# Performance work log

Hardware: AMD Instinct MI355X
Metric: run time of the kernel (lower is better)

Reference implementation:

```python
import jax, jax.numpy as jnp
import numpy as np

B, NPG, DEG = 256, 256, 8        # graphs, nodes/graph, avg degree
IN_C, HID, OUT_C = 64, 64, 64
N = B * NPG                      # 65536 nodes
E = N * DEG                      # 524288 edges
K = NPG // 2                     # ASAP ratio=0.5 -> 128 kept nodes per graph


def setup_inputs() -> dict:
    key = jax.random.key(0)
    ks = jax.random.split(key, 12)
    x = jax.random.normal(ks[0], (N, IN_C), jnp.float32)
    # within-graph random edges, no self loops (ASAP adds remaining self loops itself)
    g = jnp.arange(E) // (NPG * DEG)
    src_l = jax.random.randint(ks[1], (E,), 0, NPG)
    off = jax.random.randint(ks[2], (E,), 1, NPG)
    dst_l = (src_l + off) % NPG
    edge_index = jnp.stack([src_l + g * NPG, dst_l + g * NPG]).astype(jnp.int32)
    batch = (jnp.arange(N) // NPG).astype(jnp.int32)
    def lin(k, fi, fo):
        return jax.random.normal(k, (fi, fo), jnp.float32) / np.sqrt(fi)
    return {
        "x": x, "edge_index": edge_index, "batch": batch,
        "W1": lin(ks[3], IN_C, HID), "b1": jnp.zeros((HID,), jnp.float32),
        "lin_W": lin(ks[4], HID, HID), "lin_b": jnp.zeros((HID,), jnp.float32),
        "att_W": lin(ks[5], 2 * HID, 1), "att_b": jnp.zeros((1,), jnp.float32),
        "le1_W": lin(ks[6], HID, 1), "le1_b": jnp.zeros((1,), jnp.float32),
        "le2_W": lin(ks[7], HID, 1),
        "le3_W": lin(ks[8], HID, 1), "le3_b": jnp.zeros((1,), jnp.float32),
        "W2": lin(ks[9], HID, OUT_C), "b2": jnp.zeros((OUT_C,), jnp.float32),
    }


def reference(x, edge_index, batch, W1, b1, lin_W, lin_b, att_W, att_b,
              le1_W, le1_b, le2_W, le3_W, le3_b, W2, b2):
    src, dst = edge_index[0], edge_index[1]
    dt = x.dtype

    # ---- conv1: GCNConv(in, hid) with self loops + symmetric norm ----
    h = x @ W1
    deg = jnp.zeros((N,), dt).at[dst].add(1.0) + 1.0  # +1 self loop
    dinv = jax.lax.rsqrt(deg)
    coef = dinv[src] * dinv[dst]
    h1 = jax.ops.segment_sum(h[src] * coef[:, None], dst, N) \
         + h * (dinv * dinv)[:, None] + b1
    h1 = jax.nn.relu(h1)  # dropout is identity at inference

    # ---- ASAPooling(hid, ratio=0.5): add remaining self loops ----
    sl = jnp.arange(N)
    srcF = jnp.concatenate([src, sl])
    dstF = jnp.concatenate([dst, sl])

    x_pool_j = h1[srcF]                                   # [Ef, HID]
    x_q = jax.ops.segment_max(x_pool_j, dstF, N)          # master-node max
    x_q = (x_q @ lin_W + lin_b)[dstF]
    s = (jnp.concatenate([x_q, x_pool_j], axis=-1) @ att_W + att_b)[:, 0]
    s = jax.nn.leaky_relu(s, 0.2)
    # segment softmax over edges grouped by target
    smax = jax.ops.segment_max(s, dstF, N)
    e = jnp.exp(s - smax[dstF])
    score = e / (jax.ops.segment_sum(e, dstF, N) + 1e-16)[dstF]
    xnew = jax.ops.segment_sum(h1[srcF] * score[:, None], dstF, N)

    # fitness = sigmoid(LEConv(xnew, edges_with_self_loops))
    # LEConv: out_i = sum_{j->i}(lin1(x_j) - lin2(x_i)) + lin3(x_i)
    a = xnew @ le1_W + le1_b
    b2_ = xnew @ le2_W
    degF = jnp.zeros((N,), dt).at[dstF].add(1.0)
    fit = jax.ops.segment_sum(a[srcF], dstF, N)[:, 0] - degF * b2_[:, 0] \
          + (xnew @ le3_W + le3_b)[:, 0]
    fitness = jax.nn.sigmoid(fit)

    # top-k (ratio=0.5) per graph; equal contiguous graphs -> static shapes
    _, topi = jax.lax.top_k(fitness.reshape(B, NPG), K)   # [B, K]
    perm = (topi + jnp.arange(B)[:, None] * NPG).reshape(-1)
    x_sel = xnew[perm] * fitness[perm][:, None]           # [B*K, HID]

    # graph coarsening: A' = S^T A S (dense per graph), diag removed
    g_e = dstF // NPG
    sL = srcF - g_e * NPG
    dL = dstF - g_e * NPG
    A = jnp.zeros((B, NPG, NPG), dt).at[g_e, sL, dL].add(1.0)
    S = jnp.zeros((B, NPG, NPG), dt).at[g_e, sL, dL].add(score)
    Ssel = jnp.take_along_axis(S, topi[:, None, :], axis=2)   # [B, NPG, K]
    AS = jnp.einsum('bij,bjk->bik', A, Ssel)                  # A @ S
    A2 = jnp.einsum('bji,bjk->bik', Ssel, AS)                 # S^T (A S) -> [B,K,K]
    A2 = A2 * (1.0 - jnp.eye(K, dtype=dt))                    # remove_diag

    # ---- conv2: GCNConv(hid, out); returned edge_weight is discarded in
    # the original forward, so edges are binary (nnz of A') + self loops ----
    M = (A2 > 0).astype(dt) + jnp.eye(K, dtype=dt)            # [B, src, dst]
    h2 = (x_sel @ W2).reshape(B, K, OUT_C)
    deg2 = M.sum(axis=1)                                      # in-degree per target
    d2 = jax.lax.rsqrt(deg2)
    Mn = M * d2[:, :, None] * d2[:, None, :]
    out2 = jnp.einsum('bsd,bsf->bdf', Mn, h2) + b2            # [B, K, OUT_C]

    # ---- global_mean_pool over each graph's K kept nodes ----
    return out2.mean(axis=1)                                  # [B, OUT_C]
```

## Files before the change

kernel.cpp:

```cpp
#include <hip/hip_runtime.h>

#define NPGL 256
#define EPGL 2048
#define HIDD 64
#define KKEEP 128
#define NTH 1024

__device__ __forceinline__ int swz(int n, int c) {
  return (n << 6) + ((((c ^ n) ^ (n >> 4)) & 15) << 2);
}

__global__ void __launch_bounds__(NTH)
asap_fused(const float* __restrict__ x, const int* __restrict__ ei,
           const float* __restrict__ W1, const float* __restrict__ b1,
           const float* __restrict__ linW, const float* __restrict__ linb,
           const float* __restrict__ attW, const float* __restrict__ attb,
           const float* __restrict__ le1W, const float* __restrict__ le1b,
           const float* __restrict__ le2W,
           const float* __restrict__ le3W, const float* __restrict__ le3b,
           const float* __restrict__ W2, const float* __restrict__ b2,
           float* __restrict__ out, int Etot)
{
  const int g = blockIdx.x;
  const int tid = threadIdx.x;

  __shared__ __align__(16) float buf[NPGL * HIDD];
  __shared__ __align__(16) float mskf[4096];
  __shared__ unsigned short csrc[EPGL];
  __shared__ int rowst[NPGL + 1];
  __shared__ int cnt[NPGL];
  __shared__ float dinv_[NPGL];
  __shared__ float sA[NPGL], sB[NPGL];
  __shared__ float eself[NPGL];
  __shared__ float rsf[NPGL];
  __shared__ __align__(16) float esc[EPGL];
  __shared__ float u_[HIDD];
  __shared__ float wsum[HIDD];
  __shared__ int scanw[4];
  __shared__ float c0s;

  unsigned long long* Imask = (unsigned long long*)mskf;
  unsigned long long* Rmask = ((unsigned long long*)mskf) + 1024;
  unsigned long long* conn  = ((unsigned long long*)mskf) + 1536;
  int*   kept = (int*)(mskf + 3584);
  float* d2A  = mskf + 3712;
  float* cA   = mskf + 3840;

  const int ebase = g * EPGL;
  const int nbase = g * NPGL;

  if (tid < NPGL) cnt[tid] = 0;
  __syncthreads();

  int es[2], ed[2];
#pragma unroll
  for (int i = 0; i < 2; ++i) {
    const int e = tid + i * NTH;
    es[i] = ei[ebase + e] - nbase;
    ed[i] = ei[Etot + ebase + e] - nbase;
    atomicAdd(&cnt[ed[i]], 1);
  }

  __syncthreads();

  int vscan = 0;
  if (tid < NPGL) {
    vscan = cnt[tid];
#pragma unroll
    for (int off = 1; off < 64; off <<= 1) {
      const int up = __shfl_up(vscan, off, 64);
      if ((tid & 63) >= off) vscan += up;
    }
    if ((tid & 63) == 63) scanw[tid >> 6] = vscan;
  }
  __syncthreads();
  if (tid < NPGL) {
    int add = 0;
    const int w = tid >> 6;
    for (int ww = 0; ww < w; ++ww) add += scanw[ww];
    const int incl = vscan + add;
    rowst[tid + 1] = incl;
    cnt[tid] = incl - cnt[tid];
    if (tid == 0) rowst[0] = 0;
  }
  __syncthreads();

#pragma unroll
  for (int i = 0; i < 2; ++i) {
    const int p = atomicAdd(&cnt[ed[i]], 1);
    csrc[p] = (unsigned short)es[i];
  }
  if (tid < NPGL) {
    const int len = rowst[tid + 1] - rowst[tid];
    dinv_[tid] = rsqrtf((float)len + 1.0f);
  }
  if (tid < HIDD) {
    float a = 0.f;
    for (int f = 0; f < HIDD; ++f) a += linW[tid * HIDD + f] * attW[f];
    u_[tid] = a;
  }
  if (tid == 0) {
    float a = 0.f;
    for (int f = 0; f < HIDD; ++f) a += linb[f] * attW[f];
    c0s = a + attb[0];
  }
  {
    const float4* xg = (const float4*)(x + (size_t)nbase * HIDD);
#pragma unroll
    for (int ii = 0; ii < 4; ++ii) {
      const int i = tid + ii * NTH;
      const int r = i >> 4, c = i & 15;
      *(float4*)&buf[swz(r, c)] = xg[i];
    }
  }
  __syncthreads();

  {
    const int wv = tid >> 6;
    const int r  = ((wv & 3) << 6) + (tid & 63);
    const int fc = __builtin_amdgcn_readfirstlane(wv >> 2);
    const float* __restrict__ Wg = W1 + fc * 16;
    float4 acc[4];
#pragma unroll
    for (int c = 0; c < 4; ++c) acc[c] = make_float4(0.f, 0.f, 0.f, 0.f);
#pragma unroll
    for (int p = 0; p < 4; ++p) {
      float4 xa[4];
#pragma unroll
      for (int c = 0; c < 4; ++c) xa[c] = *(const float4*)&buf[swz(r, p * 4 + c)];
#pragma unroll
      for (int kk = 0; kk < 16; ++kk) {
        const int k = p * 16 + kk;
        const float xv = ((const float*)xa)[kk];
        const float* __restrict__ Wk = Wg + k * HIDD;
#pragma unroll
        for (int c = 0; c < 4; ++c) {
          const float4 w = *(const float4*)(Wk + c * 4);
          acc[c].x += xv * w.x; acc[c].y += xv * w.y;
          acc[c].z += xv * w.z; acc[c].w += xv * w.w;
        }
      }
    }
    __syncthreads();
#pragma unroll
    for (int c = 0; c < 4; ++c) *(float4*)&buf[swz(r, fc * 4 + c)] = acc[c];
  }
  __syncthreads();

  {
    const int d = tid >> 2, hh = tid & 3;
    const float dd = dinv_[d];
    const float sc_ = dd * dd;
    float4 acc[4];
#pragma unroll
    for (int j = 0; j < 4; ++j) {
      const int c = hh + 4 * j;
      const float4 hv = *(const float4*)&buf[swz(d, c)];
      const float4 bv = *(const float4*)&b1[4 * c];
      acc[j].x = hv.x * sc_ + bv.x; acc[j].y = hv.y * sc_ + bv.y;
      acc[j].z = hv.z * sc_ + bv.z; acc[j].w = hv.w * sc_ + bv.w;
    }
    const int s0 = rowst[d], s1 = rowst[d + 1];
    int it = s0;
    for (; it + 2 <= s1; it += 2) {
      const int sa_ = csrc[it], sb_ = csrc[it + 1];
      const float ca_ = dinv_[sa_] * dd, cb_ = dinv_[sb_] * dd;
#pragma unroll
      for (int j = 0; j < 4; ++j) {
        const float4 ha = *(const float4*)&buf[swz(sa_, hh + 4 * j)];
        const float4 hb = *(const float4*)&buf[swz(sb_, hh + 4 * j)];
        acc[j].x += ca_ * ha.x + cb_ * hb.x;
        acc[j].y += ca_ * ha.y + cb_ * hb.y;
        acc[j].z += ca_ * ha.z + cb_ * hb.z;
        acc[j].w += ca_ * ha.w + cb_ * hb.w;
      }
    }
    if (it < s1) {
      const int s = csrc[it];
      const float cf = dinv_[s] * dd;
#pragma unroll
      for (int j = 0; j < 4; ++j) {
        const float4 hv = *(const float4*)&buf[swz(s, hh + 4 * j)];
        acc[j].x += cf * hv.x; acc[j].y += cf * hv.y;
        acc[j].z += cf * hv.z; acc[j].w += cf * hv.w;
      }
    }
#pragma unroll
    for (int j = 0; j < 4; ++j) {
      acc[j].x = fmaxf(acc[j].x, 0.f); acc[j].y = fmaxf(acc[j].y, 0.f);
      acc[j].z = fmaxf(acc[j].z, 0.f); acc[j].w = fmaxf(acc[j].w, 0.f);
    }
    __syncthreads();
#pragma unroll
    for (int j = 0; j < 4; ++j) *(float4*)&buf[swz(d, hh + 4 * j)] = acc[j];
  }
  __syncthreads();

  {
    const int d = tid >> 2, hh = tid & 3;
    float4 mx[4];
    float sBp = 0.f;
#pragma unroll
    for (int j = 0; j < 4; ++j) {
      const int c = hh + 4 * j;
      const float4 hv = *(const float4*)&buf[swz(d, c)];
      mx[j] = hv;
      const float4 aw = *(const float4*)&attW[HIDD + 4 * c];
      sBp += hv.x * aw.x + hv.y * aw.y + hv.z * aw.z + hv.w * aw.w;
    }
    const int s0 = rowst[d], s1 = rowst[d + 1];
    int it = s0;
    for (; it + 2 <= s1; it += 2) {
      const int sa_ = csrc[it], sb_ = csrc[it + 1];
#pragma unroll
      for (int j = 0; j < 4; ++j) {
        const float4 ha = *(const float4*)&buf[swz(sa_, hh + 4 * j)];
        const float4 hb = *(const float4*)&buf[swz(sb_, hh + 4 * j)];
        mx[j].x = fmaxf(mx[j].x, fmaxf(ha.x, hb.x));
        mx[j].y = fmaxf(mx[j].y, fmaxf(ha.y, hb.y));
        mx[j].z = fmaxf(mx[j].z, fmaxf(ha.z, hb.z));
        mx[j].w = fmaxf(mx[j].w, fmaxf(ha.w, hb.w));
      }
    }
    if (it < s1) {
      const int s = csrc[it];
#pragma unroll
      for (int j = 0; j < 4; ++j) {
        const float4 hv = *(const float4*)&buf[swz(s, hh + 4 * j)];
        mx[j].x = fmaxf(mx[j].x, hv.x); mx[j].y = fmaxf(mx[j].y, hv.y);
        mx[j].z = fmaxf(mx[j].z, hv.z); mx[j].w = fmaxf(mx[j].w, hv.w);
      }
    }
    float sAp = 0.f;
#pragma unroll
    for (int j = 0; j < 4; ++j) {
      const float* uu = &u_[4 * (hh + 4 * j)];
      sAp += mx[j].x * uu[0] + mx[j].y * uu[1] + mx[j].z * uu[2] + mx[j].w * uu[3];
    }
    sAp += __shfl_xor(sAp, 1); sAp += __shfl_xor(sAp, 2);
    sBp += __shfl_xor(sBp, 1); sBp += __shfl_xor(sBp, 2);
    if (hh == 0) { sA[d] = c0s + sAp; sB[d] = sBp; }
  }
  __syncthreads();

  {
    const int d = tid >> 2, q = tid & 3;
    const float sa = sA[d];
    const int s0 = rowst[d], s1 = rowst[d + 1];
    float scS = sa + sB[d];
    scS = scS >= 0.f ? scS : 0.2f * scS;
    float mxv = scS;
    for (int it = s0 + q; it < s1; it += 4) {
      float sc = sa + sB[csrc[it]];
      sc = sc >= 0.f ? sc : 0.2f * sc;
      mxv = fmaxf(mxv, sc);
    }
    mxv = fmaxf(mxv, __shfl_xor(mxv, 1));
    mxv = fmaxf(mxv, __shfl_xor(mxv, 2));
    float sum = 0.f;
    for (int it = s0 + q; it < s1; it += 4) {
      float sc = sa + sB[csrc[it]];
      sc = sc >= 0.f ? sc : 0.2f * sc;
      const float e = __expf(sc - mxv);
      esc[it] = e;
      sum += e;
    }
    sum += __shfl_xor(sum, 1); sum += __shfl_xor(sum, 2);
    const float esf = __expf(scS - mxv);
    if (q == 0) {
      eself[d] = esf;
      rsf[d] = 1.0f / (esf + sum + 1e-16f);
    }
  }
  __syncthreads();

  {
    const int d = tid >> 2, hh = tid & 3;
    const float esf = eself[d];
    float4 acc[4];
#pragma unroll
    for (int j = 0; j < 4; ++j) {
      const float4 hv = *(const float4*)&buf[swz(d, hh + 4 * j)];
      acc[j].x = esf * hv.x; acc[j].y = esf * hv.y;
      acc[j].z = esf * hv.z; acc[j].w = esf * hv.w;
    }
    const int s0 = rowst[d], s1 = rowst[d + 1];
    int it = s0;
    for (; it + 2 <= s1; it += 2) {
      const int sa_ = csrc[it], sb_ = csrc[it + 1];
      const float ea = esc[it], eb = esc[it + 1];
#pragma unroll
      for (int j = 0; j < 4; ++j) {
        const float4 ha = *(const float4*)&buf[swz(sa_, hh + 4 * j)];
        const float4 hb = *(const float4*)&buf[swz(sb_, hh + 4 * j)];
        acc[j].x += ea * ha.x + eb * hb.x;
        acc[j].y += ea * ha.y + eb * hb.y;
        acc[j].z += ea * ha.z + eb * hb.z;
        acc[j].w += ea * ha.w + eb * hb.w;
      }
    }
    if (it < s1) {
      const int s = csrc[it];
      const float e = esc[it];
#pragma unroll
      for (int j = 0; j < 4; ++j) {
        const float4 hv = *(const float4*)&buf[swz(s, hh + 4 * j)];
        acc[j].x += e * hv.x; acc[j].y += e * hv.y;
        acc[j].z += e * hv.z; acc[j].w += e * hv.w;
      }
    }
    const float r = rsf[d];
#pragma unroll
    for (int j = 0; j < 4; ++j) {
      acc[j].x *= r; acc[j].y *= r; acc[j].z *= r; acc[j].w *= r;
    }
    __syncthreads();
#pragma unroll
    for (int j = 0; j < 4; ++j) *(float4*)&buf[swz(d, hh + 4 * j)] = acc[j];
  }
  __syncthreads();

  {
    const int n = tid >> 2, q = tid & 3;
    float av = 0.f, bv = 0.f, cv = 0.f;
#pragma unroll
    for (int j = 0; j < 4; ++j) {
      const int c = q + 4 * j;
      const float4 v = *(const float4*)&buf[swz(n, c)];
      const int k = c * 4;
      av += v.x * le1W[k] + v.y * le1W[k + 1] + v.z * le1W[k + 2] + v.w * le1W[k + 3];
      bv += v.x * le2W[k] + v.y * le2W[k + 1] + v.z * le2W[k + 2] + v.w * le2W[k + 3];
      cv += v.x * le3W[k] + v.y * le3W[k + 1] + v.z * le3W[k + 2] + v.w * le3W[k + 3];
    }
    av += __shfl_xor(av, 1); av += __shfl_xor(av, 2);
    bv += __shfl_xor(bv, 1); bv += __shfl_xor(bv, 2);
    cv += __shfl_xor(cv, 1); cv += __shfl_xor(cv, 2);
    if (q == 0) {
      sA[n] = av + le1b[0];
      sB[n] = bv;
      dinv_[n] = cv + le3b[0];
    }
  }
  __syncthreads();
  {
    const int d = tid >> 2, q = tid & 3;
    const int s0 = rowst[d], s1 = rowst[d + 1];
    float fp = 0.f;
    for (int it = s0 + q; it < s1; it += 4) fp += sA[csrc[it]];
    fp += __shfl_xor(fp, 1); fp += __shfl_xor(fp, 2);
    if (q == 0) {
      float f = sA[d] + fp;
      f -= (float)(s1 - s0 + 1) * sB[d];
      f += dinv_[d];
      float sg;
      if (f >= 0.f) sg = 1.f / (1.f + expf(-f));
      else { const float t = expf(f); sg = t / (1.f + t); }
      rsf[d] = sg;
    }
  }
  __syncthreads();

  {
    const int n = tid >> 2, q = tid & 3;
    const float fn = rsf[n];
    int r = 0;
    for (int m = q * 64; m < q * 64 + 64; ++m) {
      const float fm = rsf[m];
      r += ((fm > fn) || (fm == fn && m < n)) ? 1 : 0;
    }
    r += __shfl_xor(r, 1); r += __shfl_xor(r, 2);
    if (q == 0 && r < KKEEP) kept[r] = n;
  }
  __syncthreads();

  Imask[tid] = 0ull;
  __syncthreads();
  if (tid < NPGL) atomicOr(&Imask[tid * 4 + (tid >> 6)], 1ull << (tid & 63));
#pragma unroll
  for (int i = 0; i < 2; ++i)
    atomicOr(&Imask[ed[i] * 4 + (es[i] >> 6)], 1ull << (es[i] & 63));
  __syncthreads();

  if (tid < KKEEP * 4) {
    const int q = tid >> 2, w = tid & 3;
    const int kq = kept[q];
    unsigned long long acc = 0ull;
#pragma unroll
    for (int ww = 0; ww < 4; ++ww) {
      unsigned long long bits = Imask[kq * 4 + ww];
      while (bits) {
        const int m = (ww << 6) + __builtin_ctzll(bits);
        bits &= bits - 1;
        acc |= Imask[m * 4 + w];
      }
    }
    Rmask[q * 4 + w] = acc;
  }
  __syncthreads();
  if (tid < KKEEP * 2) conn[tid] = 0ull;
  __syncthreads();
  if (tid < KKEEP * 4) {
    const int p = tid >> 2, wb = tid & 3;
    const int kp = kept[p];
    const unsigned long long I0 = Imask[kp * 4 + 0], I1 = Imask[kp * 4 + 1],
                             I2 = Imask[kp * 4 + 2], I3 = Imask[kp * 4 + 3];
    unsigned long long bits = 0ull;
    for (int j = 0; j < 32; ++j) {
      const int q = wb * 32 + j;
      if (q == p) continue;
      const unsigned long long* R = &Rmask[q * 4];
      if ((I0 & R[0]) | (I1 & R[1]) | (I2 & R[2]) | (I3 & R[3]))
        bits |= 1ull << (q & 63);
    }
    atomicOr(&conn[p * 2 + (wb >> 1)], bits);
  }
  __syncthreads();

  if (tid < KKEEP) {
    const int q = tid;
    const int w = q >> 6;
    const unsigned long long bq = 1ull << (q & 63);
    int deg = 1;
    for (int p = 0; p < KKEEP; ++p) deg += (conn[p * 2 + w] & bq) ? 1 : 0;
    d2A[q] = rsqrtf((float)deg);
  }
  __syncthreads();
  if (tid < KKEEP) {
    const int s = tid;
    float acc = d2A[s];
#pragma unroll
    for (int w = 0; w < 2; ++w) {
      unsigned long long bits = conn[s * 2 + w];
      while (bits) {
        const int d = (w << 6) + __builtin_ctzll(bits);
        bits &= bits - 1;
        acc += d2A[d];
      }
    }
    cA[s] = d2A[s] * acc * rsf[kept[s]] * (1.0f / (float)KKEEP);
  }
  __syncthreads();

  {
    const int f = tid & 63, blk = tid >> 6;
    float p = 0.f;
    for (int j = 0; j < 8; ++j) {
      const int s = blk * 8 + j;
      const int ks = kept[s];
      const int off = (ks << 6) + (((((f >> 2) ^ ks) ^ (ks >> 4)) & 15) << 2) + (f & 3);
      p += cA[s] * buf[off];
    }
    esc[blk * 64 + f] = p;
  }
  __syncthreads();
  if (tid < HIDD) {
    float s = 0.f;
#pragma unroll
    for (int b = 0; b < 16; ++b) s += esc[b * 64 + tid];
    wsum[tid] = s;
  }
  __syncthreads();
  if (tid < HIDD) {
    float o = b2[tid];
    for (int k = 0; k < HIDD; ++k) o += wsum[k] * W2[k * HIDD + tid];
    out[(size_t)g * HIDD + tid] = o;
  }
}

extern "C" void kernel_launch(void* const* d_in, const int* in_sizes, int n_in,
                              void* d_out, int out_size, void* d_ws, size_t ws_size,
                              hipStream_t stream) {
  (void)n_in; (void)out_size; (void)d_ws; (void)ws_size;
  const float* x    = (const float*)d_in[0];
  const int*   ei   = (const int*)d_in[1];
  const float* W1   = (const float*)d_in[3];
  const float* b1   = (const float*)d_in[4];
  const float* linW = (const float*)d_in[5];
  const float* linb = (const float*)d_in[6];
  const float* attW = (const float*)d_in[7];
  const float* attb = (const float*)d_in[8];
  const float* le1W = (const float*)d_in[9];
  const float* le1b = (const float*)d_in[10];
  const float* le2W = (const float*)d_in[11];
  const float* le3W = (const float*)d_in[12];
  const float* le3b = (const float*)d_in[13];
  const float* W2   = (const float*)d_in[14];
  const float* b2   = (const float*)d_in[15];
  const int Etot = in_sizes[1] / 2;
  const int nGraphs = 256;

  asap_fused<<<dim3(nGraphs), dim3(NTH), 0, stream>>>(
      x, ei, W1, b1, linW, linb, attW, attb, le1W, le1b, le2W, le3W, le3b,
      W2, b2, (float*)d_out, Etot);
}
```

Baseline: 58.20 us.

## Sort nodes by in-degree for wavefront load balance and fuse softmax with aggregation

Builds a per-graph permutation of nodes ordered by in-degree through a shared-memory histogram and prefix scan. The edge-iterating phases use it so each 64-lane wavefront handles nodes with similar degrees, which cuts divergence in the per-node edge loops. It also merges the attention softmax stage with the weighted aggregation stage, dropping the eself/rsf shared round-trip and one block barrier. The cost is an extra counting-sort pass with atomics and barriers, plus an indirect perm lookup in every phase.

```diff
diff --git a/kernel.cpp b/kernel.cpp
--- a/kernel.cpp
+++ b/kernel.cpp
@@ -31,13 +31,15 @@
   __shared__ int cnt[NPGL];
   __shared__ float dinv_[NPGL];
   __shared__ float sA[NPGL], sB[NPGL];
-  __shared__ float eself[NPGL];
   __shared__ float rsf[NPGL];
   __shared__ __align__(16) float esc[EPGL];
   __shared__ float u_[HIDD];
   __shared__ float wsum[HIDD];
   __shared__ int scanw[4];
   __shared__ float c0s;
+  __shared__ int perm[NPGL];
+  __shared__ int dhist[64];
+  __shared__ int dcur[64];
 
   unsigned long long* Imask = (unsigned long long*)mskf;
   unsigned long long* Rmask = ((unsigned long long*)mskf) + 1024;
@@ -50,6 +52,7 @@
   const int nbase = g * NPGL;
 
   if (tid < NPGL) cnt[tid] = 0;
+  if (tid >= NTH - 64) dhist[tid - (NTH - 64)] = 0;
   __syncthreads();
 
   int es[2], ed[2];
@@ -60,7 +63,6 @@
     ed[i] = ei[Etot + ebase + e] - nbase;
     atomicAdd(&cnt[ed[i]], 1);
   }
-
   __syncthreads();
 
   int vscan = 0;
@@ -93,6 +95,7 @@
   if (tid < NPGL) {
     const int len = rowst[tid + 1] - rowst[tid];
     dinv_[tid] = rsqrtf((float)len + 1.0f);
+    atomicAdd(&dhist[len < 63 ? len : 63], 1);
   }
   if (tid < HIDD) {
     float a = 0.f;
@@ -147,8 +150,26 @@
   }
   __syncthreads();
 
-  {
-    const int d = tid >> 2, hh = tid & 3;
+  if (tid < 64) {
+    const int v = dhist[tid];
+    int s = v;
+#pragma unroll
+    for (int off = 1; off < 64; off <<= 1) {
+      const int up = __shfl_up(s, off, 64);
+      if (tid >= off) s += up;
+    }
+    dcur[tid] = s - v;
+  }
+  __syncthreads();
+  if (tid < NPGL) {
+    const int len = rowst[tid + 1] - rowst[tid];
+    const int b = len < 63 ? len : 63;
+    perm[atomicAdd(&dcur[b], 1)] = tid;
+  }
+  __syncthreads();
+
+  {
+    const int d = perm[tid >> 2], hh = tid & 3;
     const float dd = dinv_[d];
     const float sc_ = dd * dd;
     float4 acc[4];
@@ -197,7 +218,7 @@
   __syncthreads();
 
   {
-    const int d = tid >> 2, hh = tid & 3;
+    const int d = perm[tid >> 2], hh = tid & 3;
     float4 mx[4];
     float sBp = 0.f;
 #pragma unroll
@@ -244,13 +265,13 @@
   __syncthreads();
 
   {
-    const int d = tid >> 2, q = tid & 3;
+    const int d = perm[tid >> 2], hh = tid & 3;
     const float sa = sA[d];
     const int s0 = rowst[d], s1 = rowst[d + 1];
     float scS = sa + sB[d];
     scS = scS >= 0.f ? scS : 0.2f * scS;
     float mxv = scS;
-    for (int it = s0 + q; it < s1; it += 4) {
+    for (int it = s0 + hh; it < s1; it += 4) {
       float sc = sa + sB[csrc[it]];
       sc = sc >= 0.f ? sc : 0.2f * sc;
       mxv = fmaxf(mxv, sc);
@@ -258,7 +279,7 @@
     mxv = fmaxf(mxv, __shfl_xor(mxv, 1));
     mxv = fmaxf(mxv, __shfl_xor(mxv, 2));
     float sum = 0.f;
-    for (int it = s0 + q; it < s1; it += 4) {
+    for (int it = s0 + hh; it < s1; it += 4) {
       float sc = sa + sB[csrc[it]];
       sc = sc >= 0.f ? sc : 0.2f * sc;
       const float e = __expf(sc - mxv);
@@ -267,16 +288,8 @@
     }
     sum += __shfl_xor(sum, 1); sum += __shfl_xor(sum, 2);
     const float esf = __expf(scS - mxv);
-    if (q == 0) {
-      eself[d] = esf;
-      rsf[d] = 1.0f / (esf + sum + 1e-16f);
-    }
-  }
-  __syncthreads();
-
-  {
-    const int d = tid >> 2, hh = tid & 3;
-    const float esf = eself[d];
+    const float rs = 1.0f / (esf + sum + 1e-16f);
+
     float4 acc[4];
 #pragma unroll
     for (int j = 0; j < 4; ++j) {
@@ -284,7 +297,6 @@
       acc[j].x = esf * hv.x; acc[j].y = esf * hv.y;
       acc[j].z = esf * hv.z; acc[j].w = esf * hv.w;
     }
-    const int s0 = rowst[d], s1 = rowst[d + 1];
     int it = s0;
     for (; it + 2 <= s1; it += 2) {
       const int sa_ = csrc[it], sb_ = csrc[it + 1];
@@ -309,10 +321,9 @@
         acc[j].z += e * hv.z; acc[j].w += e * hv.w;
       }
     }
-    const float r = rsf[d];
-#pragma unroll
-    for (int j = 0; j < 4; ++j) {
-      acc[j].x *= r; acc[j].y *= r; acc[j].z *= r; acc[j].w *= r;
+#pragma unroll
+    for (int j = 0; j < 4; ++j) {
+      acc[j].x *= rs; acc[j].y *= rs; acc[j].z *= rs; acc[j].w *= rs;
     }
     __syncthreads();
 #pragma unroll
@@ -343,7 +354,7 @@
   }
   __syncthreads();
   {
-    const int d = tid >> 2, q = tid & 3;
+    const int d = perm[tid >> 2], q = tid & 3;
     const int s0 = rowst[d], s1 = rowst[d + 1];
     float fp = 0.f;
     for (int it = s0 + q; it < s1; it += 4) fp += sA[csrc[it]];
```

Result: no change. 59.34 us (+1.9%).

## Fuse ASAP attention phases and remap to 16 lanes per node

Applied to the files above, without the earlier changes.

Each node is now handled by 16 lanes with one float4 per lane instead of 4 lanes with four float4s, so neighbour-row gathers read whole contiguous 256-byte rows from LDS. The attention score, softmax and weighted aggregation are merged into one phase, with the first eight neighbour rows cached in registers and reused. Per-edge GCN coefficients are computed once during CSR construction, and the adjacency bitmask build and the x load are moved earlier to overlap with other setup. The change also simplifies the LDS swizzle, stores source indices as bytes, and drops several barriers; in exchange it uses more registers and places a barrier inside a branch on the thread index.

```diff
diff --git a/kernel.cpp b/kernel.cpp
--- a/kernel.cpp
+++ b/kernel.cpp
@@ -1,4 +1,6 @@
 #include <hip/hip_runtime.h>
+
+typedef float f4 __attribute__((ext_vector_type(4)));
 
 #define NPGL 256
 #define EPGL 2048
@@ -7,7 +9,7 @@
 #define NTH 1024
 
 __device__ __forceinline__ int swz(int n, int c) {
-  return (n << 6) + ((((c ^ n) ^ (n >> 4)) & 15) << 2);
+  return (n << 6) + (((c ^ n) & 15) << 2);
 }
 
 __global__ void __launch_bounds__(NTH)
@@ -23,17 +25,18 @@
 {
   const int g = blockIdx.x;
   const int tid = threadIdx.x;
+  const int ln = tid & 15;
+  const int grp = tid >> 4;
 
   __shared__ __align__(16) float buf[NPGL * HIDD];
   __shared__ __align__(16) float mskf[4096];
-  __shared__ unsigned short csrc[EPGL];
+  __shared__ __align__(16) float esc[EPGL];
+  __shared__ unsigned char csrc[EPGL];
   __shared__ int rowst[NPGL + 1];
   __shared__ int cnt[NPGL];
   __shared__ float dinv_[NPGL];
   __shared__ float sA[NPGL], sB[NPGL];
-  __shared__ float eself[NPGL];
   __shared__ float rsf[NPGL];
-  __shared__ __align__(16) float esc[EPGL];
   __shared__ float u_[HIDD];
   __shared__ float wsum[HIDD];
   __shared__ int scanw[4];
@@ -49,6 +52,7 @@
   const int ebase = g * EPGL;
   const int nbase = g * NPGL;
 
+  ((unsigned long long*)mskf)[tid] = 0ull;
   if (tid < NPGL) cnt[tid] = 0;
   __syncthreads();
 
@@ -60,39 +64,36 @@
     ed[i] = ei[Etot + ebase + e] - nbase;
     atomicAdd(&cnt[ed[i]], 1);
   }
-
-  __syncthreads();
-
-  int vscan = 0;
+  {
+    const f4* xg = (const f4*)(x + (size_t)nbase * HIDD);
+#pragma unroll
+    for (int ii = 0; ii < 4; ++ii) {
+      const int i = tid + ii * NTH;
+      *(f4*)&buf[swz(i >> 4, i & 15)] = xg[i];
+    }
+  }
+  __syncthreads();
+
   if (tid < NPGL) {
-    vscan = cnt[tid];
+    const int myc = cnt[tid];
+    int vscan = myc;
 #pragma unroll
     for (int off = 1; off < 64; off <<= 1) {
       const int up = __shfl_up(vscan, off, 64);
       if ((tid & 63) >= off) vscan += up;
     }
     if ((tid & 63) == 63) scanw[tid >> 6] = vscan;
-  }
-  __syncthreads();
-  if (tid < NPGL) {
+    dinv_[tid] = rsqrtf((float)myc + 1.0f);
+    __syncthreads();
     int add = 0;
     const int w = tid >> 6;
     for (int ww = 0; ww < w; ++ww) add += scanw[ww];
     const int incl = vscan + add;
     rowst[tid + 1] = incl;
-    cnt[tid] = incl - cnt[tid];
+    cnt[tid] = incl - myc;
     if (tid == 0) rowst[0] = 0;
-  }
-  __syncthreads();
-
-#pragma unroll
-  for (int i = 0; i < 2; ++i) {
-    const int p = atomicAdd(&cnt[ed[i]], 1);
-    csrc[p] = (unsigned short)es[i];
-  }
-  if (tid < NPGL) {
-    const int len = rowst[tid + 1] - rowst[tid];
-    dinv_[tid] = rsqrtf((float)len + 1.0f);
+  } else {
+    __syncthreads();
   }
   if (tid < HIDD) {
     float a = 0.f;
@@ -104,15 +105,18 @@
     for (int f = 0; f < HIDD; ++f) a += linb[f] * attW[f];
     c0s = a + attb[0];
   }
-  {
-    const float4* xg = (const float4*)(x + (size_t)nbase * HIDD);
-#pragma unroll
-    for (int ii = 0; ii < 4; ++ii) {
-      const int i = tid + ii * NTH;
-      const int r = i >> 4, c = i & 15;
-      *(float4*)&buf[swz(r, c)] = xg[i];
-    }
-  }
+  __syncthreads();
+
+#pragma unroll
+  for (int i = 0; i < 2; ++i) {
+    const int p = atomicAdd(&cnt[ed[i]], 1);
+    csrc[p] = (unsigned char)es[i];
+    esc[p] = dinv_[es[i]] * dinv_[ed[i]];
+  }
+  if (tid < NPGL) atomicOr(&Imask[tid * 4 + (tid >> 6)], 1ull << (tid & 63));
+#pragma unroll
+  for (int i = 0; i < 2; ++i)
+    atomicOr(&Imask[ed[i] * 4 + (es[i] >> 6)], 1ull << (es[i] & 63));
   __syncthreads();
 
   {
@@ -120,222 +124,155 @@
     const int r  = ((wv & 3) << 6) + (tid & 63);
     const int fc = __builtin_amdgcn_readfirstlane(wv >> 2);
     const float* __restrict__ Wg = W1 + fc * 16;
-    float4 acc[4];
-#pragma unroll
-    for (int c = 0; c < 4; ++c) acc[c] = make_float4(0.f, 0.f, 0.f, 0.f);
+    f4 acc[4];
+#pragma unroll
+    for (int c = 0; c < 4; ++c) acc[c] = f4{0.f, 0.f, 0.f, 0.f};
 #pragma unroll
     for (int p = 0; p < 4; ++p) {
-      float4 xa[4];
-#pragma unroll
-      for (int c = 0; c < 4; ++c) xa[c] = *(const float4*)&buf[swz(r, p * 4 + c)];
+      f4 xa[4];
+#pragma unroll
+      for (int c = 0; c < 4; ++c) xa[c] = *(const f4*)&buf[swz(r, p * 4 + c)];
 #pragma unroll
       for (int kk = 0; kk < 16; ++kk) {
         const int k = p * 16 + kk;
         const float xv = ((const float*)xa)[kk];
         const float* __restrict__ Wk = Wg + k * HIDD;
 #pragma unroll
-        for (int c = 0; c < 4; ++c) {
-          const float4 w = *(const float4*)(Wk + c * 4);
-          acc[c].x += xv * w.x; acc[c].y += xv * w.y;
-          acc[c].z += xv * w.z; acc[c].w += xv * w.w;
+        for (int c = 0; c < 4; ++c)
+          acc[c] += xv * *(const f4*)(Wk + c * 4);
+      }
+    }
+    __syncthreads();
+#pragma unroll
+    for (int c = 0; c < 4; ++c) *(f4*)&buf[swz(r, fc * 4 + c)] = acc[c];
+  }
+  __syncthreads();
+
+  {
+    f4 hacc[4];
+#pragma unroll
+    for (int p = 0; p < 4; ++p) {
+      const int d = (p << 6) + grp;
+      const float dd = dinv_[d];
+      const f4 own = *(const f4*)&buf[swz(d, ln)];
+      const f4 bv = *(const f4*)&b1[ln * 4];
+      f4 a = own * (dd * dd) + bv;
+      const int s0 = rowst[d], s1 = rowst[d + 1];
+      int it = s0;
+      for (; it + 2 <= s1; it += 2) {
+        const int sa_ = csrc[it], sb_ = csrc[it + 1];
+        const float ca_ = esc[it], cb_ = esc[it + 1];
+        const f4 va = *(const f4*)&buf[swz(sa_, ln)];
+        const f4 vb = *(const f4*)&buf[swz(sb_, ln)];
+        a += ca_ * va + cb_ * vb;
+      }
+      if (it < s1) {
+        const int s = csrc[it];
+        a += esc[it] * *(const f4*)&buf[swz(s, ln)];
+      }
+      a = __builtin_elementwise_max(a, f4{0.f, 0.f, 0.f, 0.f});
+      const f4 aw = *(const f4*)&attW[HIDD + ln * 4];
+      float sBp = a.x * aw.x + a.y * aw.y + a.z * aw.z + a.w * aw.w;
+      sBp += __shfl_xor(sBp, 1); sBp += __shfl_xor(sBp, 2);
+      sBp += __shfl_xor(sBp, 4); sBp += __shfl_xor(sBp, 8);
+      if (ln == 0) sB[d] = sBp;
+      hacc[p] = a;
+    }
+    __syncthreads();
+#pragma unroll
+    for (int p = 0; p < 4; ++p)
+      *(f4*)&buf[swz((p << 6) + grp, ln)] = hacc[p];
+  }
+  __syncthreads();
+
+  {
+    f4 xacc[4];
+#pragma unroll
+    for (int p = 0; p < 4; ++p) {
+      const int d = (p << 6) + grp;
+      const int s0 = rowst[d], s1 = rowst[d + 1];
+      const int deg = s1 - s0;
+      const f4 own = *(const f4*)&buf[swz(d, ln)];
+      f4 mx = own;
+      f4 cch[8];
+#pragma unroll
+      for (int j = 0; j < 8; ++j) {
+        if (j < deg) {
+          const int s = csrc[s0 + j];
+          const f4 v = *(const f4*)&buf[swz(s, ln)];
+          cch[j] = v;
+          mx = __builtin_elementwise_max(mx, v);
         }
       }
+      for (int it = s0 + 8; it < s1; ++it) {
+        const int s = csrc[it];
+        mx = __builtin_elementwise_max(mx, *(const f4*)&buf[swz(s, ln)]);
+      }
+      const f4 uu = *(const f4*)&u_[ln * 4];
+      float sAv = mx.x * uu.x + mx.y * uu.y + mx.z * uu.z + mx.w * uu.w;
+      sAv += __shfl_xor(sAv, 1); sAv += __shfl_xor(sAv, 2);
+      sAv += __shfl_xor(sAv, 4); sAv += __shfl_xor(sAv, 8);
+      const float sa = c0s + sAv;
+      float scS = sa + sB[d];
+      scS = scS >= 0.f ? scS : 0.2f * scS;
+      float mxv = scS;
+      for (int t = s0 + ln; t < s1; t += 16) {
+        float sc = sa + sB[csrc[t]];
+        sc = sc >= 0.f ? sc : 0.2f * sc;
+        mxv = fmaxf(mxv, sc);
+      }
+      mxv = fmaxf(mxv, __shfl_xor(mxv, 1));
+      mxv = fmaxf(mxv, __shfl_xor(mxv, 2));
+      mxv = fmaxf(mxv, __shfl_xor(mxv, 4));
+      mxv = fmaxf(mxv, __shfl_xor(mxv, 8));
+      float sum = 0.f;
+      for (int t = s0 + ln; t < s1; t += 16) {
+        float sc = sa + sB[csrc[t]];
+        sc = sc >= 0.f ? sc : 0.2f * sc;
+        const float e = __expf(sc - mxv);
+        esc[t] = e;
+        sum += e;
+      }
+      sum += __shfl_xor(sum, 1); sum += __shfl_xor(sum, 2);
+      sum += __shfl_xor(sum, 4); sum += __shfl_xor(sum, 8);
+      const float esf = __expf(scS - mxv);
+      const float rs = 1.0f / (esf + sum + 1e-16f);
+      asm volatile("s_waitcnt lgkmcnt(0)" ::: "memory");
+      f4 a = esf * own;
+#pragma unroll
+      for (int j = 0; j < 8; ++j) {
+        if (j < deg) a += esc[s0 + j] * cch[j];
+      }
+      for (int it = s0 + 8; it < s1; ++it) {
+        const int s = csrc[it];
+        a += esc[it] * *(const f4*)&buf[swz(s, ln)];
+      }
+      xacc[p] = a * rs;
     }
     __syncthreads();
 #pragma unroll
-    for (int c = 0; c < 4; ++c) *(float4*)&buf[swz(r, fc * 4 + c)] = acc[c];
-  }
-  __syncthreads();
-
-  {
-    const int d = tid >> 2, hh = tid & 3;
-    const float dd = dinv_[d];
-    const float sc_ = dd * dd;
-    float4 acc[4];
-#pragma unroll
-    for (int j = 0; j < 4; ++j) {
-      const int c = hh + 4 * j;
-      const float4 hv = *(const float4*)&buf[swz(d, c)];
-      const float4 bv = *(const float4*)&b1[4 * c];
-      acc[j].x = hv.x * sc_ + bv.x; acc[j].y = hv.y * sc_ + bv.y;
-      acc[j].z = hv.z * sc_ + bv.z; acc[j].w = hv.w * sc_ + bv.w;
-    }
-    const int s0 = rowst[d], s1 = rowst[d + 1];
-    int it = s0;
-    for (; it + 2 <= s1; it += 2) {
-      const int sa_ = csrc[it], sb_ = csrc[it + 1];
-      const float ca_ = dinv_[sa_] * dd, cb_ = dinv_[sb_] * dd;
-#pragma unroll
-      for (int j = 0; j < 4; ++j) {
-        const float4 ha = *(const float4*)&buf[swz(sa_, hh + 4 * j)];
-        const float4 hb = *(const float4*)&buf[swz(sb_, hh + 4 * j)];
-        acc[j].x += ca_ * ha.x + cb_ * hb.x;
-        acc[j].y += ca_ * ha.y + cb_ * hb.y;
-        acc[j].z += ca_ * ha.z + cb_ * hb.z;
-        acc[j].w += ca_ * ha.w + cb_ * hb.w;
-      }
-    }
-    if (it < s1) {
-      const int s = csrc[it];
-      const float cf = dinv_[s] * dd;
-#pragma unroll
-      for (int j = 0; j < 4; ++j) {
-        const float4 hv = *(const float4*)&buf[swz(s, hh + 4 * j)];
-        acc[j].x += cf * hv.x; acc[j].y += cf * hv.y;
-        acc[j].z += cf * hv.z; acc[j].w += cf * hv.w;
-      }
-    }
-#pragma unroll
-    for (int j = 0; j < 4; ++j) {
-      acc[j].x = fmaxf(acc[j].x, 0.f); acc[j].y = fmaxf(acc[j].y, 0.f);
-      acc[j].z = fmaxf(acc[j].z, 0.f); acc[j].w = fmaxf(acc[j].w, 0.f);
-    }
-    __syncthreads();
-#pragma unroll
-    for (int j = 0; j < 4; ++j) *(float4*)&buf[swz(d, hh + 4 * j)] = acc[j];
-  }
-  __syncthreads();
-
-  {
-    const int d = tid >> 2, hh = tid & 3;
-    float4 mx[4];
-    float sBp = 0.f;
-#pragma unroll
-    for (int j = 0; j < 4; ++j) {
-      const int c = hh + 4 * j;
-      const float4 hv = *(const float4*)&buf[swz(d, c)];
-      mx[j] = hv;
-      const float4 aw = *(const float4*)&attW[HIDD + 4 * c];
-      sBp += hv.x * aw.x + hv.y * aw.y + hv.z * aw.z + hv.w * aw.w;
-    }
-    const int s0 = rowst[d], s1 = rowst[d + 1];
-    int it = s0;
-    for (; it + 2 <= s1; it += 2) {
-      const int sa_ = csrc[it], sb_ = csrc[it + 1];
-#pragma unroll
-      for (int j = 0; j < 4; ++j) {
-        const float4 ha = *(const float4*)&buf[swz(sa_, hh + 4 * j)];
-        const float4 hb = *(const float4*)&buf[swz(sb_, hh + 4 * j)];
-        mx[j].x = fmaxf(mx[j].x, fmaxf(ha.x, hb.x));
-        mx[j].y = fmaxf(mx[j].y, fmaxf(ha.y, hb.y));
-        mx[j].z = fmaxf(mx[j].z, fmaxf(ha.z, hb.z));
-        mx[j].w = fmaxf(mx[j].w, fmaxf(ha.w, hb.w));
-      }
-    }
-    if (it < s1) {
-      const int s = csrc[it];
-#pragma unroll
-      for (int j = 0; j < 4; ++j) {
-        const float4 hv = *(const float4*)&buf[swz(s, hh + 4 * j)];
-        mx[j].x = fmaxf(mx[j].x, hv.x); mx[j].y = fmaxf(mx[j].y, hv.y);
-        mx[j].z = fmaxf(mx[j].z, hv.z); mx[j].w = fmaxf(mx[j].w, hv.w);
-      }
-    }
-    float sAp = 0.f;
-#pragma unroll
-    for (int j = 0; j < 4; ++j) {
-      const float* uu = &u_[4 * (hh + 4 * j)];
-      sAp += mx[j].x * uu[0] + mx[j].y * uu[1] + mx[j].z * uu[2] + mx[j].w * uu[3];
-    }
-    sAp += __shfl_xor(sAp, 1); sAp += __shfl_xor(sAp, 2);
-    sBp += __shfl_xor(sBp, 1); sBp += __shfl_xor(sBp, 2);
-    if (hh == 0) { sA[d] = c0s + sAp; sB[d] = sBp; }
-  }
-  __syncthreads();
-
-  {
-    const int d = tid >> 2, q = tid & 3;
-    const float sa = sA[d];
-    const int s0 = rowst[d], s1 = rowst[d + 1];
-    float scS = sa + sB[d];
-    scS = scS >= 0.f ? scS : 0.2f * scS;
-    float mxv = scS;
-    for (int it = s0 + q; it < s1; it += 4) {
-      float sc = sa + sB[csrc[it]];
-      sc = sc >= 0.f ? sc : 0.2f * sc;
-      mxv = fmaxf(mxv, sc);
-    }
-    mxv = fmaxf(mxv, __shfl_xor(mxv, 1));
-    mxv = fmaxf(mxv, __shfl_xor(mxv, 2));
-    float sum = 0.f;
-    for (int it = s0 + q; it < s1; it += 4) {
-      float sc = sa + sB[csrc[it]];
-      sc = sc >= 0.f ? sc : 0.2f * sc;
-      const float e = __expf(sc - mxv);
-      esc[it] = e;
-      sum += e;
-    }
-    sum += __shfl_xor(sum, 1); sum += __shfl_xor(sum, 2);
-    const float esf = __expf(scS - mxv);
-    if (q == 0) {
-      eself[d] = esf;
-      rsf[d] = 1.0f / (esf + sum + 1e-16f);
-    }
-  }
-  __syncthreads();
-
-  {
-    const int d = tid >> 2, hh = tid & 3;
-    const float esf = eself[d];
-    float4 acc[4];
-#pragma unroll
-    for (int j = 0; j < 4; ++j) {
-      const float4 hv = *(const float4*)&buf[swz(d, hh + 4 * j)];
-      acc[j].x = esf * hv.x; acc[j].y = esf * hv.y;
-      acc[j].z = esf * hv.z; acc[j].w = esf * hv.w;
-    }
-    const int s0 = rowst[d], s1 = rowst[d + 1];
-    int it = s0;
-    for (; it + 2 <= s1; it += 2) {
-      const int sa_ = csrc[it], sb_ = csrc[it + 1];
-      const float ea = esc[it], eb = esc[it + 1];
-#pragma unroll
-      for (int j = 0; j < 4; ++j) {
-        const float4 ha = *(const float4*)&buf[swz(sa_, hh + 4 * j)];
-        const float4 hb = *(const float4*)&buf[swz(sb_, hh + 4 * j)];
-        acc[j].x += ea * ha.x + eb * hb.x;
-        acc[j].y += ea * ha.y + eb * hb.y;
-        acc[j].z += ea * ha.z + eb * hb.z;
-        acc[j].w += ea * ha.w + eb * hb.w;
-      }
-    }
-    if (it < s1) {
-      const int s = csrc[it];
-      const float e = esc[it];
-#pragma unroll
-      for (int j = 0; j < 4; ++j) {
-        const float4 hv = *(const float4*)&buf[swz(s, hh + 4 * j)];
-        acc[j].x += e * hv.x; acc[j].y += e * hv.y;
-        acc[j].z += e * hv.z; acc[j].w += e * hv.w;
-      }
-    }
-    const float r = rsf[d];
-#pragma unroll
-    for (int j = 0; j < 4; ++j) {
-      acc[j].x *= r; acc[j].y *= r; acc[j].z *= r; acc[j].w *= r;
-    }
-    __syncthreads();
-#pragma unroll
-    for (int j = 0; j < 4; ++j) *(float4*)&buf[swz(d, hh + 4 * j)] = acc[j];
-  }
-  __syncthreads();
-
-  {
-    const int n = tid >> 2, q = tid & 3;
-    float av = 0.f, bv = 0.f, cv = 0.f;
-#pragma unroll
-    for (int j = 0; j < 4; ++j) {
-      const int c = q + 4 * j;
-      const float4 v = *(const float4*)&buf[swz(n, c)];
-      const int k = c * 4;
-      av += v.x * le1W[k] + v.y * le1W[k + 1] + v.z * le1W[k + 2] + v.w * le1W[k + 3];
-      bv += v.x * le2W[k] + v.y * le2W[k + 1] + v.z * le2W[k + 2] + v.w * le2W[k + 3];
-      cv += v.x * le3W[k] + v.y * le3W[k + 1] + v.z * le3W[k + 2] + v.w * le3W[k + 3];
-    }
+    for (int p = 0; p < 4; ++p)
+      *(f4*)&buf[swz((p << 6) + grp, ln)] = xacc[p];
+  }
+  __syncthreads();
+
+#pragma unroll
+  for (int p = 0; p < 4; ++p) {
+    const int n = (p << 6) + grp;
+    const f4 v = *(const f4*)&buf[swz(n, ln)];
+    const f4 w1v = *(const f4*)&le1W[ln * 4];
+    const f4 w2v = *(const f4*)&le2W[ln * 4];
+    const f4 w3v = *(const f4*)&le3W[ln * 4];
+    float av = v.x * w1v.x + v.y * w1v.y + v.z * w1v.z + v.w * w1v.w;
+    float bv = v.x * w2v.x + v.y * w2v.y + v.z * w2v.z + v.w * w2v.w;
+    float cv = v.x * w3v.x + v.y * w3v.y + v.z * w3v.z + v.w * w3v.w;
     av += __shfl_xor(av, 1); av += __shfl_xor(av, 2);
+    av += __shfl_xor(av, 4); av += __shfl_xor(av, 8);
     bv += __shfl_xor(bv, 1); bv += __shfl_xor(bv, 2);
+    bv += __shfl_xor(bv, 4); bv += __shfl_xor(bv, 8);
     cv += __shfl_xor(cv, 1); cv += __shfl_xor(cv, 2);
-    if (q == 0) {
+    cv += __shfl_xor(cv, 4); cv += __shfl_xor(cv, 8);
+    if (ln == 0) {
       sA[n] = av + le1b[0];
       sB[n] = bv;
       dinv_[n] = cv + le3b[0];
@@ -373,14 +310,6 @@
   }
   __syncthreads();
 
-  Imask[tid] = 0ull;
-  __syncthreads();
-  if (tid < NPGL) atomicOr(&Imask[tid * 4 + (tid >> 6)], 1ull << (tid & 63));
-#pragma unroll
-  for (int i = 0; i < 2; ++i)
-    atomicOr(&Imask[ed[i] * 4 + (es[i] >> 6)], 1ull << (es[i] & 63));
-  __syncthreads();
-
   if (tid < KKEEP * 4) {
     const int q = tid >> 2, w = tid & 3;
     const int kq = kept[q];
@@ -447,7 +376,7 @@
     for (int j = 0; j < 8; ++j) {
       const int s = blk * 8 + j;
       const int ks = kept[s];
-      const int off = (ks << 6) + (((((f >> 2) ^ ks) ^ (ks >> 4)) & 15) << 2) + (f & 3);
+      const int off = (ks << 6) + ((((f >> 2) ^ ks) & 15) << 2) + (f & 3);
       p += cA[s] * buf[off];
     }
     esc[blk * 64 + f] = p;
```

New measurement: 67.19 us. 1.15x slower.
